# Optimization experiments

Hardware: AMD Instinct MI355X
Metric: run time of the kernel (lower is better)

Reference implementation:

```python
import jax, jax.numpy as jnp
import numpy as np
import math

EPS = 1e-6


def setup_inputs() -> dict:
    key = jax.random.key(0)
    k1, k2, k3 = jax.random.split(key, 3)
    B, S, D = 8, 2048, 256
    return {
        "query": jax.random.normal(k1, (B, S, D), dtype=jnp.float32),
        "keys": jax.random.normal(k2, (B, S, D), dtype=jnp.float32),
        "values": jax.random.normal(k3, (B, S, D), dtype=jnp.float32),
        "c": jnp.asarray(0.01, dtype=jnp.float32),  # learned curvature parameter
    }


def reference(query, keys, values, c):
    # query/keys: [B,S,D], values: [B,S,Dv]
    scale = math.sqrt(query.shape[-1])
    q2 = jnp.sum(query * query, axis=-1)            # [B,S]  |q_i|^2
    k2 = jnp.sum(keys * keys, axis=-1)              # [B,S]  |k_j|^2
    cross = jnp.einsum("bid,bjd->bij", query, keys)  # [B,S,S]
    # squared pairwise distance via identity, avoiding the [B,S,S,D] diff tensor
    nd2 = jnp.maximum(q2[:, :, None] + k2[:, None, :] - 2.0 * cross, 0.0)
    # faithful to original: denom pairs query row i with key row i (broadcast quirk)
    denom = jnp.maximum((1.0 - c * q2) * (1.0 - c * k2), EPS)  # [B,S]
    arg = jnp.maximum(1.0 + 2.0 * c * nd2 / denom[:, :, None], 1.0 + EPS)
    dist = jnp.arccosh(arg)                          # [B,S,S]
    attn = jax.nn.softmax(-dist / scale, axis=-1)
    return jnp.einsum("bij,bjd->bid", attn, values)
```

## Files before the change

### kernel.cpp

```cpp
#include <hip/hip_runtime.h>

#define B_N   8
#define S_LEN 2048
#define D_DIM 256

typedef __attribute__((ext_vector_type(4)))  float          f32x4;
typedef __attribute__((ext_vector_type(16))) float          f32x16;
typedef __attribute__((ext_vector_type(8)))  short          s16x8;
typedef __attribute__((ext_vector_type(8)))  __bf16         b16x8;
typedef __attribute__((ext_vector_type(8)))  unsigned short u16x8;
typedef __attribute__((ext_vector_type(4)))  unsigned int   u32x4;

__device__ __forceinline__ unsigned short f2bf(float f) {
    unsigned u = __builtin_bit_cast(unsigned, f);
    u += 0x7FFFu + ((u >> 16) & 1u);
    return (unsigned short)(u >> 16);
}
__device__ __forceinline__ u16x8 pack8(f32x4 a, f32x4 b) {
    u16x8 o;
#pragma unroll
    for (int u = 0; u < 4; ++u) { o[u] = f2bf(a[u]); o[u + 4] = f2bf(b[u]); }
    return o;
}
__device__ __forceinline__ f32x16 zero16() {
    f32x16 z;
#pragma unroll
    for (int i = 0; i < 16; ++i) z[i] = 0.f;
    return z;
}
__device__ __forceinline__ unsigned cvtpk(float lo, float hi) {
    unsigned r;
    asm("v_cvt_pk_bf16_f32 %0, %1, %2" : "=v"(r) : "v"(lo), "v"(hi));
    return r;
}
__device__ __forceinline__ void xswap(unsigned& x, unsigned& y, int lh) {
    unsigned vs = lh ? x : y;
    unsigned vr = (unsigned)__shfl_xor((int)vs, 32, 64);
    x = lh ? vr : x;
    y = lh ? y : vr;
}
__device__ __forceinline__ float hw_sqrt(float x) {
    float r; asm("v_sqrt_f32 %0, %1" : "=v"(r) : "v"(x)); return r;
}
__device__ __forceinline__ float hw_log2(float x) {
    float r; asm("v_log_f32 %0, %1" : "=v"(r) : "v"(x)); return r;
}
__device__ __forceinline__ float hw_exp2(float x) {
    float r; asm("v_exp_f32 %0, %1" : "=v"(r) : "v"(x)); return r;
}
__device__ __forceinline__ float hw_rcp(float x) {
    float r; asm("v_rcp_f32 %0, %1" : "=v"(r) : "v"(x)); return r;
}
__device__ __forceinline__ void gload16(const void* g, void* l) {
    __builtin_amdgcn_global_load_lds((const __attribute__((address_space(1))) void*)g,
                                     (__attribute__((address_space(3))) void*)l, 16, 0, 0);
}

template <typename A>
__device__ __forceinline__ auto mfma3216_(A a, A b, f32x16 c, int)
    -> decltype(__builtin_amdgcn_mfma_f32_32x32x16_bf16(a, b, c, 0, 0, 0)) {
    return __builtin_amdgcn_mfma_f32_32x32x16_bf16(a, b, c, 0, 0, 0);
}
template <typename A>
__device__ __forceinline__ f32x16 mfma3216_(A a, A b, f32x16 c, long) {
    b16x8 a2 = __builtin_bit_cast(b16x8, a);
    b16x8 b2 = __builtin_bit_cast(b16x8, b);
    return __builtin_amdgcn_mfma_f32_32x32x16_bf16(a2, b2, c, 0, 0, 0);
}
__device__ __forceinline__ f32x16 MFMA(u16x8 a, u16x8 b, f32x16 c) {
    return mfma3216_(__builtin_bit_cast(s16x8, a), __builtin_bit_cast(s16x8, b), c, 0);
}

__global__ void __launch_bounds__(256) prep_rows(const float* __restrict__ Q,
                                                 const float* __restrict__ K,
                                                 const float* __restrict__ cp,
                                                 float* __restrict__ q2g,
                                                 float* __restrict__ k2g,
                                                 float* __restrict__ cfg) {
    const int w = threadIdx.x >> 6, l = threadIdx.x & 63;
    const float c = *cp;
#pragma unroll 1
    for (int p = 0; p < 16; ++p) {
        const int row = blockIdx.x * 64 + p * 4 + w;
        f32x4 qv = *((const f32x4*)(Q + (size_t)row * D_DIM) + l);
        f32x4 kv = *((const f32x4*)(K + (size_t)row * D_DIM) + l);
        float sq = qv[0]*qv[0] + qv[1]*qv[1] + qv[2]*qv[2] + qv[3]*qv[3];
        float sk = kv[0]*kv[0] + kv[1]*kv[1] + kv[2]*kv[2] + kv[3]*kv[3];
#pragma unroll
        for (int m = 1; m < 64; m <<= 1) {
            sq += __shfl_xor(sq, m, 64);
            sk += __shfl_xor(sk, m, 64);
        }
        if (l == 0) {
            q2g[row] = sq;
            k2g[row] = sk;
            float dn = fmaxf((1.f - c * sq) * (1.f - c * sk), 1e-6f);
            cfg[row] = 2.f * c / dn;
        }
    }
}

__global__ void __launch_bounds__(256) cvt_bf16(const float* __restrict__ src,
                                                unsigned short* __restrict__ dst) {
    const size_t i = ((size_t)blockIdx.x * 256 + threadIdx.x) * 8;
    f32x4 a = *(const f32x4*)(src + i);
    f32x4 b = *(const f32x4*)(src + i + 4);
    *(u16x8*)(dst + i) = pack8(a, b);
}

__global__ void __launch_bounds__(256) transp_v(const float* __restrict__ V,
                                                unsigned short* __restrict__ VT) {
    __shared__ float tile[64][65];
    const int bid = blockIdx.x;
    const int b = bid >> 7, rem = bid & 127, jt = rem >> 2, dt = rem & 3;
    const int j0 = jt * 64, d0 = dt * 64;
    const int t = threadIdx.x;
#pragma unroll
    for (int p = 0; p < 4; ++p) {
        const int jr = p * 16 + (t >> 4);
        f32x4 v = *(const f32x4*)(V + (size_t)(b * S_LEN + j0 + jr) * D_DIM + d0 + (t & 15) * 4);
#pragma unroll
        for (int u = 0; u < 4; ++u) tile[jr][(t & 15) * 4 + u] = v[u];
    }
    __syncthreads();
#pragma unroll
    for (int p = 0; p < 2; ++p) {
        const int dr = p * 32 + (t >> 3), seg = t & 7;
        u16x8 o;
#pragma unroll
        for (int u = 0; u < 8; ++u) o[u] = f2bf(tile[seg * 8 + u][dr]);
        *(u16x8*)(VT + (size_t)(b * D_DIM + d0 + dr) * S_LEN + j0 + seg * 8) = o;
    }
}

template <int PRE>
__global__ void __launch_bounds__(256, 2) hyp_attn(
    const float* __restrict__ Qf, const float* __restrict__ Kf, const float* __restrict__ Vf,
    const unsigned short* __restrict__ Kb, const unsigned short* __restrict__ VTg,
    const float* __restrict__ q2g, const float* __restrict__ k2g, const float* __restrict__ cfg,
    float* __restrict__ out) {
    __shared__ __align__(1024) unsigned char tiles[65536];
    __shared__ float k2sh[S_LEN];
    __shared__ float lsumBuf[2][2][32];
    const int bid = blockIdx.x;
    const int nb = (bid & 7) * 64 + (bid >> 3);
    const int b = nb >> 6, rt = nb & 63;
    const int tid = threadIdx.x;
    const int w = tid >> 6, l = tid & 63;
    const int l31 = l & 31, lh = l >> 5;
    const int jsub = w & 1, dh = w >> 1;
    const int qr0 = rt * 32;
    const int qrow = b * S_LEN + qr0 + l31;

    *(f32x4*)&k2sh[tid * 8]     = *(const f32x4*)(k2g + b * S_LEN + tid * 8);
    *(f32x4*)&k2sh[tid * 8 + 4] = *(const f32x4*)(k2g + b * S_LEN + tid * 8 + 4);

    u16x8 qf[16];
    {
        const float* qp = Qf + (size_t)qrow * D_DIM + lh * 8;
#pragma unroll
        for (int ks = 0; ks < 16; ++ks) {
            f32x4 a = *(const f32x4*)(qp + ks * 16);
            f32x4 c4 = *(const f32x4*)(qp + ks * 16 + 4);
            qf[ks] = pack8(a, c4);
        }
    }
    const float q2r = q2g[qrow];
    const float cfr = cfg[qrow];
    const float base1 = fmaf(cfr, q2r, 1.0f);

    f32x16 oacc[4];
#pragma unroll
    for (int i = 0; i < 4; ++i) oacc[i] = zero16();
    float lsum = 0.f;

    const size_t kbBase = (size_t)b * S_LEN * D_DIM;

    auto stageK = [&](int it) {
        const int j0 = it * 64;
#pragma unroll
        for (int p = 0; p < 8; ++p) {
            const int idx = p * 256 + tid;
            const int row = idx >> 5, sl = idx & 31;
            const unsigned short* gp = Kb + kbBase + (size_t)(j0 + row) * D_DIM
                                     + ((sl ^ (row & 7)) << 3);
            gload16(gp, (char*)tiles + idx * 16);
        }
    };
    auto stageV = [&](int it) {
        const int j0 = it * 64;
#pragma unroll
        for (int p = 0; p < 8; ++p) {
            const int idx = p * 256 + tid;
            const int d = idx >> 3, sl = idx & 7;
            const unsigned short* gp = VTg + ((size_t)b * D_DIM + d) * S_LEN + j0
                                     + ((sl ^ (d & 7)) << 3);
            gload16(gp, (char*)tiles + 32768 + idx * 16);
        }
    };
    auto stageK0 = [&](int it) {
        const int j0 = it * 64;
#pragma unroll
        for (int p = 0; p < 8; ++p) {
            const int idx = p * 256 + tid;
            const int row = idx >> 5, sl = idx & 31;
            const float* sp = Kf + kbBase + (size_t)(j0 + row) * D_DIM
                            + ((sl ^ (row & 7)) << 3);
            *(u16x8*)((char*)tiles + idx * 16) =
                pack8(*(const f32x4*)sp, *(const f32x4*)(sp + 4));
        }
    };
    auto stageV0 = [&](int it) {
        const int j0 = it * 64;
#pragma unroll
        for (int p = 0; p < 8; ++p) {
            const int idx = p * 256 + tid;
            const int d = idx >> 3, sl = idx & 7;
            const int jj = (sl ^ (d & 7)) << 3;
            u16x8 o;
#pragma unroll
            for (int u = 0; u < 8; ++u)
                o[u] = f2bf(Vf[kbBase + (size_t)(j0 + jj + u) * D_DIM + d]);
            *(u16x8*)((char*)tiles + 32768 + idx * 16) = o;
        }
    };

    const int xk = (l31 & 7) << 4;
    const char* KBp = (const char*)tiles + (jsub * 32 + l31) * 512;
    const char* VBp = (const char*)tiles + 32768 + (dh * 128 + l31) * 128;

    if (PRE) {
        stageK(0);
        asm volatile("s_waitcnt vmcnt(0) lgkmcnt(0)" ::: "memory");
        __builtin_amdgcn_s_barrier();
    }

#pragma unroll 1
    for (int it = 0; it < 32; ++it) {
        if (PRE) {
            stageV(it);
        } else {
            stageK0(it); stageV0(it);
            __syncthreads();
        }

        f32x16 sacc = zero16();
#pragma unroll
        for (int ks = 0; ks < 16; ++ks) {
            u16x8 kf = *(const u16x8*)(KBp + (((ks * 2 + lh) << 4) ^ xk));
            sacc = MFMA(kf, qf[ks], sacc);
        }

        if (PRE) {
            asm volatile("s_waitcnt vmcnt(0)" ::: "memory");
            __builtin_amdgcn_s_barrier();
            if (it < 31) stageK(it + 1);
        }

        f32x4 k2q[4];
#pragma unroll
        for (int g = 0; g < 4; ++g)
            k2q[g] = *(const f32x4*)&k2sh[it * 64 + jsub * 32 + g * 8 + lh * 4];
#pragma unroll
        for (int r = 0; r < 16; ++r) {
            const float t = fmaf(-2.f, sacc[r], k2q[r >> 2][r & 3]);
            const float arg = fmaxf(fmaf(cfr, t, base1), 1.f + 1e-6f);
            const float y = arg + hw_sqrt(fmaf(arg, arg, -1.f));
            const float p = hw_exp2(hw_log2(y) * -0.0625f);
            lsum += p;
            sacc[r] = p;
        }
        unsigned A_ = cvtpk(sacc[0], sacc[1]),   C_ = cvtpk(sacc[2], sacc[3]);
        unsigned Bv = cvtpk(sacc[4], sacc[5]),   D_ = cvtpk(sacc[6], sacc[7]);
        unsigned E_ = cvtpk(sacc[8], sacc[9]),   G_ = cvtpk(sacc[10], sacc[11]);
        unsigned F_ = cvtpk(sacc[12], sacc[13]), H_ = cvtpk(sacc[14], sacc[15]);
        xswap(A_, Bv, lh); xswap(C_, D_, lh);
        xswap(E_, F_, lh); xswap(G_, H_, lh);
        const u16x8 pa0 = __builtin_bit_cast(u16x8, (u32x4){A_, C_, Bv, D_});
        const u16x8 pa1 = __builtin_bit_cast(u16x8, (u32x4){E_, G_, F_, H_});

#pragma unroll
        for (int db = 0; db < 4; ++db) {
            u16x8 vf0 = *(const u16x8*)(VBp + db * 4096 +
                                        (((jsub * 4 + lh) << 4) ^ xk));
            oacc[db] = MFMA(pa0, vf0, oacc[db]);
            u16x8 vf1 = *(const u16x8*)(VBp + db * 4096 +
                                        (((jsub * 4 + 2 + lh) << 4) ^ xk));
            oacc[db] = MFMA(pa1, vf1, oacc[db]);
        }

        if (PRE) {
            asm volatile("s_waitcnt vmcnt(0)" ::: "memory");
            __builtin_amdgcn_s_barrier();
        } else {
            __syncthreads();
        }
    }

    lsum += __shfl_xor(lsum, 32, 64);
    if (lh == 0) lsumBuf[jsub][dh][l31] = lsum;
    float* sf = (float*)tiles;
    if (jsub == 1) {
#pragma unroll
        for (int db = 0; db < 4; ++db)
#pragma unroll
            for (int r = 0; r < 16; ++r) {
                const int crow = (r & 3) + 8 * (r >> 2) + 4 * lh;
                sf[dh * 4096 + crow * 128 + db * 32 + l31] = oacc[db][r];
            }
    }
    __syncthreads();
    if (jsub == 0) {
        float rdn[16];
#pragma unroll
        for (int r = 0; r < 16; ++r) {
            const int crow = (r & 3) + 8 * (r >> 2) + 4 * lh;
            rdn[r] = hw_rcp(lsumBuf[0][dh][crow] + lsumBuf[1][dh][crow]);
        }
#pragma unroll
        for (int db = 0; db < 4; ++db)
#pragma unroll
            for (int r = 0; r < 16; ++r) {
                const int crow = (r & 3) + 8 * (r >> 2) + 4 * lh;
                const float o = oacc[db][r] + sf[dh * 4096 + crow * 128 + db * 32 + l31];
                out[(size_t)(b * S_LEN + qr0 + crow) * D_DIM + dh * 128 + db * 32 + l31]
                    = o * rdn[r];
            }
    }
}

extern "C" void kernel_launch(void* const* d_in, const int* in_sizes, int n_in,
                              void* d_out, int out_size, void* d_ws, size_t ws_size,
                              hipStream_t stream) {
    const float* Q = (const float*)d_in[0];
    const float* K = (const float*)d_in[1];
    const float* V = (const float*)d_in[2];
    const float* cp = (const float*)d_in[3];
    float* out = (float*)d_out;
    (void)in_sizes; (void)n_in; (void)out_size;

    const size_t BS = (size_t)B_N * S_LEN;
    float* q2g = (float*)d_ws;
    float* k2g = q2g + BS;
    float* cfg = k2g + BS;
    unsigned short* Kb = (unsigned short*)(cfg + BS);
    unsigned short* VTg = Kb + BS * D_DIM;
    const size_t need_full = 3 * BS * 4 + 2 * BS * D_DIM * 2;

    prep_rows<<<(B_N * S_LEN) / 64, 256, 0, stream>>>(Q, K, cp, q2g, k2g, cfg);

    if (ws_size >= need_full) {
        cvt_bf16<<<(int)((BS * D_DIM / 8) / 256), 256, 0, stream>>>(K, Kb);
        transp_v<<<B_N * (S_LEN / 64) * (D_DIM / 64), 256, 0, stream>>>(V, VTg);
        hyp_attn<1><<<512, 256, 0, stream>>>(Q, K, V, Kb, VTg, q2g, k2g, cfg, out);
    } else {
        hyp_attn<0><<<512, 256, 0, stream>>>(Q, K, V, Kb, VTg, q2g, k2g, cfg, out);
    }
}
```

Measured before the change: 120.5 us.

## Split hyperbolic-distance elementwise work between paired waves via LDS exchange

Two waves (dh=0 and dh=1) previously computed the same 32x32 score tile redundantly, each applying the full arccosh/exp transform to all 16 accumulator elements. Now each wave transforms only half (8 elements), packs them to bf16, and swaps halves with its partner wave through a small LDS buffer. The row-sum normalisation now adds all four partial sums. It also raises wave priority around the MFMA loops. The cost is an extra LDS round trip and a barrier placed mid-iteration, which may stall the pipeline.

```diff
diff --git a/kernel.cpp b/kernel.cpp
--- a/kernel.cpp
+++ b/kernel.cpp
@@ -142,6 +142,7 @@
     __shared__ __align__(1024) unsigned char tiles[65536];
     __shared__ float k2sh[S_LEN];
     __shared__ float lsumBuf[2][2][32];
+    __shared__ __align__(16) unsigned PexBuf[4][64][4];
     const int bid = blockIdx.x;
     const int nb = (bid & 7) * 64 + (bid >> 3);
     const int b = nb >> 6, rt = nb & 63;
@@ -149,6 +150,7 @@
     const int w = tid >> 6, l = tid & 63;
     const int l31 = l & 31, lh = l >> 5;
     const int jsub = w & 1, dh = w >> 1;
+    const int rb = dh * 8;
     const int qr0 = rt * 32;
     const int qrow = b * S_LEN + qr0 + l31;
 
@@ -244,41 +246,48 @@
             __syncthreads();
         }
 
+        __builtin_amdgcn_s_setprio(1);
         f32x16 sacc = zero16();
 #pragma unroll
         for (int ks = 0; ks < 16; ++ks) {
             u16x8 kf = *(const u16x8*)(KBp + (((ks * 2 + lh) << 4) ^ xk));
             sacc = MFMA(kf, qf[ks], sacc);
         }
-
-        if (PRE) {
-            asm volatile("s_waitcnt vmcnt(0)" ::: "memory");
-            __builtin_amdgcn_s_barrier();
-            if (it < 31) stageK(it + 1);
-        }
-
-        f32x4 k2q[4];
-#pragma unroll
-        for (int g = 0; g < 4; ++g)
-            k2q[g] = *(const f32x4*)&k2sh[it * 64 + jsub * 32 + g * 8 + lh * 4];
-#pragma unroll
-        for (int r = 0; r < 16; ++r) {
-            const float t = fmaf(-2.f, sacc[r], k2q[r >> 2][r & 3]);
+        __builtin_amdgcn_s_setprio(0);
+
+        f32x4 kk0 = *(const f32x4*)&k2sh[it * 64 + jsub * 32 + (dh * 2) * 8 + lh * 4];
+        f32x4 kk1 = *(const f32x4*)&k2sh[it * 64 + jsub * 32 + (dh * 2 + 1) * 8 + lh * 4];
+
+        float pv[8];
+#pragma unroll
+        for (int i = 0; i < 8; ++i) {
+            const float k2j = (i < 4 ? kk0 : kk1)[i & 3];
+            const float t = fmaf(-2.f, sacc[rb + i], k2j);
             const float arg = fmaxf(fmaf(cfr, t, base1), 1.f + 1e-6f);
             const float y = arg + hw_sqrt(fmaf(arg, arg, -1.f));
             const float p = hw_exp2(hw_log2(y) * -0.0625f);
             lsum += p;
-            sacc[r] = p;
-        }
-        unsigned A_ = cvtpk(sacc[0], sacc[1]),   C_ = cvtpk(sacc[2], sacc[3]);
-        unsigned Bv = cvtpk(sacc[4], sacc[5]),   D_ = cvtpk(sacc[6], sacc[7]);
-        unsigned E_ = cvtpk(sacc[8], sacc[9]),   G_ = cvtpk(sacc[10], sacc[11]);
-        unsigned F_ = cvtpk(sacc[12], sacc[13]), H_ = cvtpk(sacc[14], sacc[15]);
-        xswap(A_, Bv, lh); xswap(C_, D_, lh);
-        xswap(E_, F_, lh); xswap(G_, H_, lh);
-        const u16x8 pa0 = __builtin_bit_cast(u16x8, (u32x4){A_, C_, Bv, D_});
-        const u16x8 pa1 = __builtin_bit_cast(u16x8, (u32x4){E_, G_, F_, H_});
-
+            pv[i] = p;
+        }
+        unsigned X0 = cvtpk(pv[0], pv[1]), X1 = cvtpk(pv[2], pv[3]);
+        unsigned X2 = cvtpk(pv[4], pv[5]), X3 = cvtpk(pv[6], pv[7]);
+        xswap(X0, X2, lh); xswap(X1, X3, lh);
+        const u32x4 own = {X0, X1, X2, X3};
+        *(u32x4*)&PexBuf[w][l][0] = own;
+
+        if (PRE) {
+            asm volatile("s_waitcnt vmcnt(0) lgkmcnt(0)" ::: "memory");
+            __builtin_amdgcn_s_barrier();
+            if (it < 31) stageK(it + 1);
+        } else {
+            __syncthreads();
+        }
+
+        const u32x4 oth = *(const u32x4*)&PexBuf[w ^ 2][l][0];
+        const u16x8 pa0 = __builtin_bit_cast(u16x8, dh ? oth : own);
+        const u16x8 pa1 = __builtin_bit_cast(u16x8, dh ? own : oth);
+
+        __builtin_amdgcn_s_setprio(1);
 #pragma unroll
         for (int db = 0; db < 4; ++db) {
             u16x8 vf0 = *(const u16x8*)(VBp + db * 4096 +
@@ -288,6 +297,7 @@
                                         (((jsub * 4 + 2 + lh) << 4) ^ xk));
             oacc[db] = MFMA(pa1, vf1, oacc[db]);
         }
+        __builtin_amdgcn_s_setprio(0);
 
         if (PRE) {
             asm volatile("s_waitcnt vmcnt(0)" ::: "memory");
@@ -315,7 +325,8 @@
 #pragma unroll
         for (int r = 0; r < 16; ++r) {
             const int crow = (r & 3) + 8 * (r >> 2) + 4 * lh;
-            rdn[r] = hw_rcp(lsumBuf[0][dh][crow] + lsumBuf[1][dh][crow]);
+            rdn[r] = hw_rcp(lsumBuf[0][0][crow] + lsumBuf[0][1][crow] +
+                            lsumBuf[1][0][crow] + lsumBuf[1][1][crow]);
         }
 #pragma unroll
         for (int db = 0; db < 4; ++db)
```

After: 129.1 us. 1.07x slower.

## Load V fragments directly to registers and double-buffer K tiles in LDS

Applied to the files above, without the earlier changes.

V tiles no longer go through LDS. Each lane loads its bf16 V^T fragments straight from global memory into registers for the PV MFMAs. The freed LDS half becomes a second K buffer, so the next K tile is prefetched at the start of each iteration and the mid-iteration barrier goes away. This cuts LDS traffic and one barrier per iteration, but adds register pressure and uncoalesced-ish per-lane global loads whose latency must now hide behind the QK MFMAs and the exp math.

```diff
diff --git a/kernel.cpp b/kernel.cpp
--- a/kernel.cpp
+++ b/kernel.cpp
@@ -176,7 +176,7 @@
 
     const size_t kbBase = (size_t)b * S_LEN * D_DIM;
 
-    auto stageK = [&](int it) {
+    auto stageK = [&](int buf, int it) {
         const int j0 = it * 64;
 #pragma unroll
         for (int p = 0; p < 8; ++p) {
@@ -184,21 +184,10 @@
             const int row = idx >> 5, sl = idx & 31;
             const unsigned short* gp = Kb + kbBase + (size_t)(j0 + row) * D_DIM
                                      + ((sl ^ (row & 7)) << 3);
-            gload16(gp, (char*)tiles + idx * 16);
+            gload16(gp, (char*)tiles + buf * 32768 + idx * 16);
         }
     };
-    auto stageV = [&](int it) {
-        const int j0 = it * 64;
-#pragma unroll
-        for (int p = 0; p < 8; ++p) {
-            const int idx = p * 256 + tid;
-            const int d = idx >> 3, sl = idx & 7;
-            const unsigned short* gp = VTg + ((size_t)b * D_DIM + d) * S_LEN + j0
-                                     + ((sl ^ (d & 7)) << 3);
-            gload16(gp, (char*)tiles + 32768 + idx * 16);
-        }
-    };
-    auto stageK0 = [&](int it) {
+    auto stageK0 = [&](int buf, int it) {
         const int j0 = it * 64;
 #pragma unroll
         for (int p = 0; p < 8; ++p) {
@@ -206,55 +195,62 @@
             const int row = idx >> 5, sl = idx & 31;
             const float* sp = Kf + kbBase + (size_t)(j0 + row) * D_DIM
                             + ((sl ^ (row & 7)) << 3);
-            *(u16x8*)((char*)tiles + idx * 16) =
+            *(u16x8*)((char*)tiles + buf * 32768 + idx * 16) =
                 pack8(*(const f32x4*)sp, *(const f32x4*)(sp + 4));
         }
     };
-    auto stageV0 = [&](int it) {
-        const int j0 = it * 64;
-#pragma unroll
-        for (int p = 0; p < 8; ++p) {
-            const int idx = p * 256 + tid;
-            const int d = idx >> 3, sl = idx & 7;
-            const int jj = (sl ^ (d & 7)) << 3;
-            u16x8 o;
-#pragma unroll
-            for (int u = 0; u < 8; ++u)
-                o[u] = f2bf(Vf[kbBase + (size_t)(j0 + jj + u) * D_DIM + d]);
-            *(u16x8*)((char*)tiles + 32768 + idx * 16) = o;
+    const unsigned short* vbase = VTg + ((size_t)(b * D_DIM + dh * 128 + l31) * S_LEN)
+                                + jsub * 32 + lh * 8;
+    auto loadVg = [&](int it, u16x8 (&Vr)[8]) {
+        const unsigned short* p0 = vbase + it * 64;
+#pragma unroll
+        for (int db = 0; db < 4; ++db) {
+            Vr[db * 2]     = *(const u16x8*)(p0 + (size_t)(db * 32) * S_LEN);
+            Vr[db * 2 + 1] = *(const u16x8*)(p0 + (size_t)(db * 32) * S_LEN + 16);
+        }
+    };
+    auto loadV0 = [&](int it, u16x8 (&Vr)[8]) {
+        const int j0 = it * 64 + jsub * 32 + lh * 8;
+#pragma unroll
+        for (int db = 0; db < 4; ++db) {
+            const int d = dh * 128 + db * 32 + l31;
+            u16x8 o0, o1;
+#pragma unroll
+            for (int u = 0; u < 8; ++u) {
+                o0[u] = f2bf(Vf[kbBase + (size_t)(j0 + u) * D_DIM + d]);
+                o1[u] = f2bf(Vf[kbBase + (size_t)(j0 + 16 + u) * D_DIM + d]);
+            }
+            Vr[db * 2] = o0; Vr[db * 2 + 1] = o1;
         }
     };
 
     const int xk = (l31 & 7) << 4;
     const char* KBp = (const char*)tiles + (jsub * 32 + l31) * 512;
-    const char* VBp = (const char*)tiles + 32768 + (dh * 128 + l31) * 128;
 
     if (PRE) {
-        stageK(0);
+        stageK(0, 0);
         asm volatile("s_waitcnt vmcnt(0) lgkmcnt(0)" ::: "memory");
         __builtin_amdgcn_s_barrier();
     }
 
 #pragma unroll 1
     for (int it = 0; it < 32; ++it) {
+        const int kb = it & 1;
+        u16x8 VA[8];
         if (PRE) {
-            stageV(it);
+            loadVg(it, VA);
+            if (it < 31) stageK(kb ^ 1, it + 1);
         } else {
-            stageK0(it); stageV0(it);
+            stageK0(kb, it);
+            loadV0(it, VA);
             __syncthreads();
         }
 
         f32x16 sacc = zero16();
 #pragma unroll
         for (int ks = 0; ks < 16; ++ks) {
-            u16x8 kf = *(const u16x8*)(KBp + (((ks * 2 + lh) << 4) ^ xk));
+            u16x8 kf = *(const u16x8*)(KBp + kb * 32768 + (((ks * 2 + lh) << 4) ^ xk));
             sacc = MFMA(kf, qf[ks], sacc);
-        }
-
-        if (PRE) {
-            asm volatile("s_waitcnt vmcnt(0)" ::: "memory");
-            __builtin_amdgcn_s_barrier();
-            if (it < 31) stageK(it + 1);
         }
 
         f32x4 k2q[4];
@@ -281,12 +277,8 @@
 
 #pragma unroll
         for (int db = 0; db < 4; ++db) {
-            u16x8 vf0 = *(const u16x8*)(VBp + db * 4096 +
-                                        (((jsub * 4 + lh) << 4) ^ xk));
-            oacc[db] = MFMA(pa0, vf0, oacc[db]);
-            u16x8 vf1 = *(const u16x8*)(VBp + db * 4096 +
-                                        (((jsub * 4 + 2 + lh) << 4) ^ xk));
-            oacc[db] = MFMA(pa1, vf1, oacc[db]);
+            oacc[db] = MFMA(pa0, VA[db * 2], oacc[db]);
+            oacc[db] = MFMA(pa1, VA[db * 2 + 1], oacc[db]);
         }
 
         if (PRE) {
```

After: 125.4 us. 4.1% more time.
